# Performance work log

Hardware: AMD Instinct MI355X
Metric: run time of the kernel (lower is better)

The kernel has to match this reference:

```python
import jax, jax.numpy as jnp
import numpy as np

RHO = 10.0
TAU = 0.1


def setup_inputs() -> dict:
    key = jax.random.key(0)
    k1, k2 = jax.random.split(key)
    N, D, C = 8192, 512, 128
    embeddings = jax.random.normal(k1, (N, D), dtype=jnp.float32)
    classes = jax.random.randint(k2, (N,), 0, C, dtype=jnp.int64)
    return {"embeddings": embeddings, "classes": classes}


def reference(embeddings, classes):
    n = embeddings.shape[0]
    dt = embeddings.dtype

    # calculate_similarities_pt: cosine similarity (dot products of L2-normalized embeddings)
    norms = jnp.linalg.norm(embeddings, axis=1, keepdims=True)
    normed = embeddings / jnp.maximum(norms, jnp.asarray(1e-12, dt))
    dot_products = jnp.einsum("nd,md->nm", normed, normed)  # [N, N]

    # calculate_groups_pt: same-class mask (excluding self) and different-class mask
    eq = classes[:, None] == classes[None, :]
    eye = jnp.eye(n, dtype=bool)
    same_group = (eq & ~eye).astype(dt)       # [N, N]
    different_group = (~eq).astype(dt)        # [N, N]

    # diagonal gets factor -RHO -> strongly negative score, effectively masked out
    raw_scores = ((same_group + different_group) * (1.0 + RHO) - RHO) * dot_products / TAU
    max_raw_score = jnp.max(raw_scores, axis=1, keepdims=True)
    shifted_scores = jnp.exp(raw_scores - max_raw_score)

    shifted_positive_scores = same_group * shifted_scores
    sum_shifted_negative_scores = jnp.sum(different_group * shifted_scores, axis=1, keepdims=True)

    denom = shifted_positive_scores + sum_shifted_negative_scores
    # safe_division: 0 where denominator is 0
    ratio = jnp.where(denom > 0, shifted_positive_scores / jnp.where(denom > 0, denom, 1.0), 0.0)
    # safe_log: 0 where argument is 0 (masked by same_group anyway)
    log_ratio = jnp.where(ratio > 0, jnp.log(jnp.where(ratio > 0, ratio, 1.0)), 0.0)
    infonce_losses = -log_ratio * same_group

    num_pos = jnp.sum(same_group)
    loss = jnp.where(num_pos > 0, jnp.sum(infonce_losses) / jnp.where(num_pos > 0, num_pos, 1.0), 0.0)
    return loss
```

## Files before the change

### kernel.cpp

```cpp
#include <hip/hip_runtime.h>
#include <hip/hip_bf16.h>


constexpr int   D      = 512;
constexpr int   BT     = 128;
constexpr int   BK     = 128;
constexpr int   NSTEP  = D / BK;
constexpr float SHIFTL = 14.4269504088896340f;
constexpr float QS2L   = 10.0f * 1.4426950408889634f / 16129.0f;
constexpr float LN2    = 0.6931471805599453f;

typedef __attribute__((ext_vector_type(4))) int i32x4;
typedef unsigned char uchar;
typedef unsigned long ulong_t;

__device__ inline void gload_lds16(const uchar* g, void* l) {
    __builtin_amdgcn_global_load_lds(
        (const __attribute__((address_space(1))) void*)g,
        (__attribute__((address_space(3))) void*)l, 16, 0, 0);
}

__global__ void k_normalize(const float* __restrict__ emb,
                            const int* __restrict__ classes,
                            uchar* __restrict__ normed,
                            int* __restrict__ hist, int n) {
    if (blockIdx.x == 0) {
        __shared__ int h[128];
        if (threadIdx.x < 128) h[threadIdx.x] = 0;
        __syncthreads();
        for (int i = threadIdx.x; i < n; i += 256)
            atomicAdd(&h[classes[i] & 127], 1);
        __syncthreads();
        if (threadIdx.x < 128) hist[threadIdx.x] = h[threadIdx.x];
    }
    int row  = blockIdx.x * 4 + (threadIdx.x >> 6);
    int lane = threadIdx.x & 63;
    if (row >= n) return;
    const float4* src = (const float4*)(emb + (size_t)row * D);
    float4 a = src[lane * 2];
    float4 b = src[lane * 2 + 1];
    float ss = a.x*a.x + a.y*a.y + a.z*a.z + a.w*a.w
             + b.x*b.x + b.y*b.y + b.z*b.z + b.w*b.w;
#pragma unroll
    for (int m = 1; m < 64; m <<= 1) ss += __shfl_xor(ss, m, 64);
    float sc = 127.0f / fmaxf(sqrtf(ss), 1e-12f);
    union { signed char c[8]; ulong_t u; } o;
    float v[8] = {a.x, a.y, a.z, a.w, b.x, b.y, b.z, b.w};
#pragma unroll
    for (int k = 0; k < 8; ++k) {
        int q = (int)rintf(v[k] * sc);
        q = q > 127 ? 127 : (q < -127 ? -127 : q);
        o.c[k] = (signed char)q;
    }
    *(ulong_t*)&normed[(size_t)row * D + lane * 8] = o.u;
}

__global__ __launch_bounds__(256, 3) void k_zgemm(
    const uchar* __restrict__ normed, const int* __restrict__ classes,
    float* __restrict__ Zpart, int n, int nb, int npairs) {
    __shared__ char ring[3][16384];
    __shared__ int clsrow[BT], clscol[BT];

    const int tid  = threadIdx.x;
    const int lane = tid & 63;
    const int w    = tid >> 6;
    const int l15  = lane & 15, l4 = lane >> 4;
    const size_t QS = (size_t)64 * n;

    int q8 = npairs >> 3, r8 = npairs & 7;
    int xcd = blockIdx.x & 7, off = blockIdx.x >> 3;
    int orig = (xcd < r8 ? xcd * (q8 + 1) : r8 * (q8 + 1) + (xcd - r8) * q8) + off;

    const int sgrid = nb >> 3;
    int idx = orig, si = 0;
    for (;;) { int rc = 36 + (sgrid - 1 - si) * 64; if (idx < rc) break; idx -= rc; ++si; }
    int bi, bj;
    if (idx < 36) { int u = 0, rem = 8; while (idx >= rem) { idx -= rem; ++u; --rem; }
                    bi = si * 8 + u; bj = si * 8 + u + idx; }
    else { idx -= 36; int sj = si + 1 + (idx >> 6); int v = idx & 63;
           bi = si * 8 + (v >> 3); bj = sj * 8 + (v & 7); }
    const int row0 = bi * BT, c0 = bj * BT;
    const bool diagblk = (bi == bj);

    if (tid < BT) clsrow[tid] = classes[row0 + tid];
    else          clscol[tid - BT] = classes[c0 + tid - BT];

    i32x4 areg[2][8];
#pragma unroll
    for (int rg = 0; rg < 2; ++rg)
#pragma unroll
        for (int kf = 0; kf < 8; ++kf)
            areg[rg][kf] = *(const i32x4*)&normed[
                (size_t)(row0 + w * 32 + rg * 16 + l15) * D + kf * 64 + l4 * 16];

    const int src16 = (lane & 3) ^ ((lane >> 3) & 3);
    size_t gB[2]; int lo[2];
#pragma unroll
    for (int it = 0; it < 2; ++it) {
        int chunk = w * 2 + it;
        int row   = chunk * 16 + (lane >> 2);
        gB[it] = (size_t)(c0 + row) * D + src16 * 16;
        lo[it] = chunk * 1024;
    }
    char* ringb = &ring[0][0];

    auto STAGE = [&](int sbo, int kk) {
#pragma unroll
        for (int h = 0; h < 2; ++h)
#pragma unroll
            for (int it = 0; it < 2; ++it)
                gload_lds16(normed + gB[it] + kk + h * 64,
                            ringb + sbo + h * 8192 + lo[it]);
    };

    i32x4 acc[2][8];
#pragma unroll
    for (int rg = 0; rg < 2; ++rg)
#pragma unroll
        for (int cf = 0; cf < 8; ++cf) acc[rg][cf] = (i32x4){0, 0, 0, 0};

    STAGE(0, 0);
    STAGE(16384, BK);
    __builtin_amdgcn_sched_barrier(0);
    asm volatile("s_waitcnt vmcnt(4) lgkmcnt(0)" ::: "memory");
    __builtin_amdgcn_s_barrier();
    __builtin_amdgcn_sched_barrier(0);

    const int rsw = (l15 >> 1) & 3;

#pragma unroll
    for (int kt = 0; kt < NSTEP; ++kt) {
        const int cur = kt % 3;
        if (kt + 2 < NSTEP) STAGE(((kt + 2) % 3) * 16384, (kt + 2) * BK);
        const char* base = ringb + cur * 16384;
#pragma unroll
        for (int h = 0; h < 2; ++h) {
            const char* lb = base + h * 8192;
            i32x4 bfr[8];
#pragma unroll
            for (int cf = 0; cf < 8; ++cf) {
                int rb = cf * 16 + l15;
                bfr[cf] = *(const i32x4*)(lb + rb * 64 + ((l4 ^ rsw) << 4));
            }
            __builtin_amdgcn_s_setprio(1);
#pragma unroll
            for (int rg = 0; rg < 2; ++rg)
#pragma unroll
                for (int cf = 0; cf < 8; ++cf)
                    acc[rg][cf] = __builtin_amdgcn_mfma_i32_16x16x64_i8(
                        areg[rg][kt * 2 + h], bfr[cf], acc[rg][cf], 0, 0, 0);
            __builtin_amdgcn_s_setprio(0);
        }
        __builtin_amdgcn_sched_barrier(0);
        if (kt + 2 < NSTEP)       asm volatile("s_waitcnt vmcnt(4)" ::: "memory");
        else if (kt + 2 == NSTEP) asm volatile("s_waitcnt vmcnt(0)" ::: "memory");
        if (kt + 1 < NSTEP) {
            __builtin_amdgcn_s_barrier();
            __builtin_amdgcn_sched_barrier(0);
        }
    }
    __syncthreads();

    float* redr = (float*)ringb;
    float* redc = (float*)(ringb + 2048);

    int crow[2][4];
#pragma unroll
    for (int rg = 0; rg < 2; ++rg)
#pragma unroll
        for (int r = 0; r < 4; ++r)
            crow[rg][r] = clsrow[w * 32 + rg * 16 + l4 * 4 + r];
    int ccv[8];
#pragma unroll
    for (int cf = 0; cf < 8; ++cf) ccv[cf] = clscol[cf * 16 + l15];

    float cq[8][3];
#pragma unroll
    for (int cf = 0; cf < 8; ++cf) cq[cf][0] = cq[cf][1] = cq[cf][2] = 0.f;

#pragma unroll
    for (int rg = 0; rg < 2; ++rg) {
#pragma unroll
        for (int r = 0; r < 4; ++r) {
            int rr = w * 32 + rg * 16 + l4 * 4 + r;
            int cr = crow[rg][r];
            float z = 0.f, ns = 0.f, p1 = 0.f;
#pragma unroll
            for (int cf = 0; cf < 8; ++cf) {
                int cc = cf * 16 + l15;
                float tt = fmaf((float)acc[rg][cf][r], QS2L, -SHIFTL);
                float e = exp2f(tt);
                bool same = (cr == ccv[cf]);
                bool dg   = diagblk && (rr == cc);
                if (!same) { z += e; cq[cf][0] += e; }
                else if (!dg) { ns += tt; p1 += e; cq[cf][1] += tt; cq[cf][2] += e; }
            }
#pragma unroll
            for (int m = 1; m < 16; m <<= 1) {
                z  += __shfl_xor(z,  m, 16);
                ns += __shfl_xor(ns, m, 16);
                p1 += __shfl_xor(p1, m, 16);
            }
            if (l15 == 0) {
                redr[rr * 3 + 0] = z;
                redr[rr * 3 + 1] = ns;
                redr[rr * 3 + 2] = p1;
            }
        }
    }
    if (!diagblk) {
#pragma unroll
        for (int cf = 0; cf < 8; ++cf) {
            float z = cq[cf][0], nsv = cq[cf][1], p = cq[cf][2];
            z += __shfl_xor(z, 16, 64);  z += __shfl_xor(z, 32, 64);
            nsv += __shfl_xor(nsv, 16, 64); nsv += __shfl_xor(nsv, 32, 64);
            p += __shfl_xor(p, 16, 64);  p += __shfl_xor(p, 32, 64);
            if (l4 == 0) {
                float* pp = &redc[(w * 128 + cf * 16 + l15) * 3];
                pp[0] = z; pp[1] = nsv; pp[2] = p;
            }
        }
    }
    __syncthreads();

    if (tid < BT) {
#pragma unroll
        for (int q = 0; q < 3; ++q)
            Zpart[q * QS + (size_t)bj * n + row0 + tid] = redr[tid * 3 + q];
    } else if (!diagblk) {
        int cc = tid - BT;
#pragma unroll
        for (int q = 0; q < 3; ++q)
            Zpart[q * QS + (size_t)bi * n + c0 + cc] =
                redc[(0 * 128 + cc) * 3 + q] + redc[(1 * 128 + cc) * 3 + q] +
                redc[(2 * 128 + cc) * 3 + q] + redc[(3 * 128 + cc) * 3 + q];
    }
}

__global__ void k_rowterms(const float* __restrict__ Zpart,
                           const int* __restrict__ classes,
                           const int* __restrict__ hist,
                           float* __restrict__ partial, int n) {
    const int tid = threadIdx.x;
    const int i   = blockIdx.x * 128 + tid;
    const size_t QS = (size_t)64 * n;
    float z = 0.f, ns = 0.f, p1 = 0.f;
    for (int s = 0; s < 64; ++s) {
        size_t o = (size_t)s * n + i;
        z  += Zpart[o];
        ns += Zpart[QS + o];
        p1 += Zpart[2 * QS + o];
    }
    float c    = (float)(hist[classes[i] & 127] - 1);
    float loss = -ns * LN2 + c * logf(z) + p1 / z;

    __shared__ float sl[2], sc[2];
    float L = loss, C = c;
#pragma unroll
    for (int m = 1; m < 64; m <<= 1) {
        L += __shfl_xor(L, m, 64);
        C += __shfl_xor(C, m, 64);
    }
    if ((tid & 63) == 0) { sl[tid >> 6] = L; sc[tid >> 6] = C; }
    __syncthreads();
    if (tid == 0) {
        partial[blockIdx.x * 2]     = sl[0] + sl[1];
        partial[blockIdx.x * 2 + 1] = sc[0] + sc[1];
    }
}

__global__ void k_final(const float* __restrict__ partial,
                        float* __restrict__ out) {
    int lane = threadIdx.x;
    float L = partial[lane * 2];
    float C = partial[lane * 2 + 1];
#pragma unroll
    for (int m = 1; m < 64; m <<= 1) {
        L += __shfl_xor(L, m, 64);
        C += __shfl_xor(C, m, 64);
    }
    if (lane == 0) out[0] = (C > 0.f) ? L / C : 0.f;
}

extern "C" void kernel_launch(void* const* d_in, const int* in_sizes, int n_in,
                              void* d_out, int out_size, void* d_ws, size_t ws_size,
                              hipStream_t stream) {
    const float* emb     = (const float*)d_in[0];
    const int*   classes = (const int*)d_in[1];
    float*       out     = (float*)d_out;
    const int n  = in_sizes[1];
    const int nb = n / BT;
    const int npairs = nb * (nb + 1) / 2;

    uchar*  normed  = (uchar*)d_ws;
    float*  Zpart   = (float*)((char*)d_ws + (size_t)n * D);
    float*  partial = Zpart + (size_t)3 * 64 * n;
    int*    hist    = (int*)(partial + 128);

    k_normalize<<<n / 4, 256, 0, stream>>>(emb, classes, normed, hist, n);
    k_zgemm<<<npairs, 256, 0, stream>>>(normed, classes, Zpart, n, nb, npairs);
    k_rowterms<<<n / 128, 128, 0, stream>>>(Zpart, classes, hist, partial, n);
    k_final<<<1, 64, 0, stream>>>(partial, out);
}
```

Before: 73.53 us.

## Load B fragments directly from global into registers, dropping LDS ring pipeline

New measurement: 114.1 us. 1.55x slower.

```diff
diff --git a/kernel.cpp b/kernel.cpp
--- a/kernel.cpp
+++ b/kernel.cpp
@@ -4,8 +4,6 @@
 
 constexpr int   D      = 512;
 constexpr int   BT     = 128;
-constexpr int   BK     = 128;
-constexpr int   NSTEP  = D / BK;
 constexpr float SHIFTL = 14.4269504088896340f;
 constexpr float QS2L   = 10.0f * 1.4426950408889634f / 16129.0f;
 constexpr float LN2    = 0.6931471805599453f;
@@ -13,12 +11,6 @@
 typedef __attribute__((ext_vector_type(4))) int i32x4;
 typedef unsigned char uchar;
 typedef unsigned long ulong_t;
-
-__device__ inline void gload_lds16(const uchar* g, void* l) {
-    __builtin_amdgcn_global_load_lds(
-        (const __attribute__((address_space(1))) void*)g,
-        (__attribute__((address_space(3))) void*)l, 16, 0, 0);
-}
 
 __global__ void k_normalize(const float* __restrict__ emb,
                             const int* __restrict__ classes,
@@ -55,10 +47,11 @@
     *(ulong_t*)&normed[(size_t)row * D + lane * 8] = o.u;
 }
 
-__global__ __launch_bounds__(256, 3) void k_zgemm(
+__global__ __launch_bounds__(256, 2) void k_zgemm(
     const uchar* __restrict__ normed, const int* __restrict__ classes,
     float* __restrict__ Zpart, int n, int nb, int npairs) {
-    __shared__ char ring[3][16384];
+    __shared__ float redr[BT * 3];
+    __shared__ float redc[4 * BT * 3];
     __shared__ int clsrow[BT], clscol[BT];
 
     const int tid  = threadIdx.x;
@@ -93,25 +86,8 @@
             areg[rg][kf] = *(const i32x4*)&normed[
                 (size_t)(row0 + w * 32 + rg * 16 + l15) * D + kf * 64 + l4 * 16];
 
-    const int src16 = (lane & 3) ^ ((lane >> 3) & 3);
-    size_t gB[2]; int lo[2];
-#pragma unroll
-    for (int it = 0; it < 2; ++it) {
-        int chunk = w * 2 + it;
-        int row   = chunk * 16 + (lane >> 2);
-        gB[it] = (size_t)(c0 + row) * D + src16 * 16;
-        lo[it] = chunk * 1024;
-    }
-    char* ringb = &ring[0][0];
-
-    auto STAGE = [&](int sbo, int kk) {
-#pragma unroll
-        for (int h = 0; h < 2; ++h)
-#pragma unroll
-            for (int it = 0; it < 2; ++it)
-                gload_lds16(normed + gB[it] + kk + h * 64,
-                            ringb + sbo + h * 8192 + lo[it]);
-    };
+    const uchar* bbase = normed + (size_t)c0 * D + (size_t)l15 * D + l4 * 16;
+#define BADDR(KF, CF) ((const i32x4*)(bbase + (size_t)(CF) * 16 * D + (KF) * 64))
 
     i32x4 acc[2][8];
 #pragma unroll
@@ -119,50 +95,28 @@
 #pragma unroll
         for (int cf = 0; cf < 8; ++cf) acc[rg][cf] = (i32x4){0, 0, 0, 0};
 
-    STAGE(0, 0);
-    STAGE(16384, BK);
-    __builtin_amdgcn_sched_barrier(0);
-    asm volatile("s_waitcnt vmcnt(4) lgkmcnt(0)" ::: "memory");
-    __builtin_amdgcn_s_barrier();
-    __builtin_amdgcn_sched_barrier(0);
-
-    const int rsw = (l15 >> 1) & 3;
-
-#pragma unroll
-    for (int kt = 0; kt < NSTEP; ++kt) {
-        const int cur = kt % 3;
-        if (kt + 2 < NSTEP) STAGE(((kt + 2) % 3) * 16384, (kt + 2) * BK);
-        const char* base = ringb + cur * 16384;
-#pragma unroll
-        for (int h = 0; h < 2; ++h) {
-            const char* lb = base + h * 8192;
-            i32x4 bfr[8];
-#pragma unroll
-            for (int cf = 0; cf < 8; ++cf) {
-                int rb = cf * 16 + l15;
-                bfr[cf] = *(const i32x4*)(lb + rb * 64 + ((l4 ^ rsw) << 4));
-            }
-            __builtin_amdgcn_s_setprio(1);
-#pragma unroll
-            for (int rg = 0; rg < 2; ++rg)
-#pragma unroll
-                for (int cf = 0; cf < 8; ++cf)
-                    acc[rg][cf] = __builtin_amdgcn_mfma_i32_16x16x64_i8(
-                        areg[rg][kt * 2 + h], bfr[cf], acc[rg][cf], 0, 0, 0);
-            __builtin_amdgcn_s_setprio(0);
-        }
-        __builtin_amdgcn_sched_barrier(0);
-        if (kt + 2 < NSTEP)       asm volatile("s_waitcnt vmcnt(4)" ::: "memory");
-        else if (kt + 2 == NSTEP) asm volatile("s_waitcnt vmcnt(0)" ::: "memory");
-        if (kt + 1 < NSTEP) {
-            __builtin_amdgcn_s_barrier();
-            __builtin_amdgcn_sched_barrier(0);
-        }
-    }
-    __syncthreads();
-
-    float* redr = (float*)ringb;
-    float* redc = (float*)(ringb + 2048);
+    i32x4 b0[8], b1[8];
+#pragma unroll
+    for (int cf = 0; cf < 8; ++cf) b0[cf] = *BADDR(0, cf);
+
+#define STEP(KF, BCUR, BNXT)                                                   \
+    if ((KF) + 1 < 8) {                                                        \
+        _Pragma("unroll") for (int cf = 0; cf < 8; ++cf)                       \
+            BNXT[cf] = *BADDR((KF) + 1, cf);                                   \
+    }                                                                          \
+    __builtin_amdgcn_s_setprio(1);                                             \
+    _Pragma("unroll") for (int cf = 0; cf < 8; ++cf) {                         \
+        acc[0][cf] = __builtin_amdgcn_mfma_i32_16x16x64_i8(                    \
+            areg[0][KF], BCUR[cf], acc[0][cf], 0, 0, 0);                       \
+        acc[1][cf] = __builtin_amdgcn_mfma_i32_16x16x64_i8(                    \
+            areg[1][KF], BCUR[cf], acc[1][cf], 0, 0, 0);                       \
+    }                                                                          \
+    __builtin_amdgcn_s_setprio(0);
+
+    STEP(0, b0, b1) STEP(1, b1, b0) STEP(2, b0, b1) STEP(3, b1, b0)
+    STEP(4, b0, b1) STEP(5, b1, b0) STEP(6, b0, b1) STEP(7, b1, b0)
+#undef STEP
+#undef BADDR
 
     int crow[2][4];
 #pragma unroll
```
